# Optimization experiments

Measured on AMD Instinct MI355X. Metric: run time of the kernel, lower is better.

The kernel has to match this reference:

```python
import jax, jax.numpy as jnp
import numpy as np

N = 30000      # num nodes (cells)
E = 480000     # num edges (avg degree 16)
D_IN = 1000    # input_dim (genes)
H = 8          # nheads
F_H = 32       # hidden_dim per head
D_EMB = 64     # embedding_dim
NEG_SLOPE = 0.2


def setup_inputs() -> dict:
    key = jax.random.key(0)
    ks = jax.random.split(key, 12)
    glorot = lambda k, shape, fan: (jax.random.normal(k, shape, jnp.float32)
                                    * (1.0 / np.sqrt(fan)))
    return {
        "x": jax.random.normal(ks[0], (N, D_IN), jnp.float32),
        "edge_index": jax.random.randint(ks[1], (2, E), 0, N),
        "edge_weight": jax.random.uniform(ks[2], (E,), jnp.float32),
        # GATConv params
        "W": glorot(ks[3], (D_IN, H * F_H), D_IN),
        "att_src": glorot(ks[4], (H, F_H), F_H),
        "att_dst": glorot(ks[5], (H, F_H), F_H),
        "bias_gat": jnp.zeros((H * F_H,), jnp.float32),
        # embedding Linear
        "emb_W": glorot(ks[6], (H * F_H, D_EMB), H * F_H),
        "emb_b": jnp.zeros((D_EMB,), jnp.float32),
        # decoder MLP
        "dec_W1": glorot(ks[7], (D_EMB, F_H), D_EMB),
        "dec_b1": jnp.zeros((F_H,), jnp.float32),
        "dec_W2": glorot(ks[8], (F_H, D_IN), F_H),
        "dec_b2": jnp.zeros((D_IN,), jnp.float32),
    }


def _gat_conv(x, edge_index, W, att_src, att_dst, bias):
    n = x.shape[0]
    h = (x @ W).reshape(n, H, F_H)                    # [N,H,F]
    a_s = jnp.einsum('nhf,hf->nh', h, att_src)        # [N,H]
    a_d = jnp.einsum('nhf,hf->nh', h, att_dst)        # [N,H]
    # add self loops (PyG default add_self_loops=True)
    loops = jnp.arange(n)
    src = jnp.concatenate([edge_index[0], loops])     # [E+N]
    dst = jnp.concatenate([edge_index[1], loops])     # [E+N]
    logits = jax.nn.leaky_relu(a_s[src] + a_d[dst], NEG_SLOPE)  # [E+N,H]
    # segment softmax over incoming edges of each destination node
    m = jax.ops.segment_max(logits, dst, num_segments=n)        # [N,H]
    p = jnp.exp(logits - m[dst])
    denom = jax.ops.segment_sum(p, dst, num_segments=n)         # [N,H]
    alpha = p / denom[dst]                                      # [E+N,H]
    msg = h[src] * alpha[:, :, None]                            # [E+N,H,F]
    out = jax.ops.segment_sum(msg, dst, num_segments=n)         # [N,H,F]
    return out.reshape(n, H * F_H) + bias


def reference(x, edge_index, edge_weight, W, att_src, att_dst, bias_gat,
              emb_W, emb_b, dec_W1, dec_b1, dec_W2, dec_b2):
    # edge_weight is accepted but unused: PyG GATConv with edge_dim=None has
    # no edge-feature pathway.
    h = jax.nn.relu(_gat_conv(x, edge_index, W, att_src, att_dst, bias_gat))
    z = h @ emb_W + emb_b                               # [N, D_EMB]
    d = jax.nn.relu(z @ dec_W1 + dec_b1)                # [N, F_H]
    recon = d @ dec_W2 + dec_b2                         # [N, D_IN]
    return recon, z
```

## Files before the change

kernel.cpp:

```cpp
#include <hip/hip_runtime.h>
#include <hip/hip_bf16.h>

#define N_NODES 30000
#define N_EDGES 480000
#define D_IN    1000
#define KPAD    1024
#define NHEAD   8
#define F_HID   32
#define D_EMB   64
#define NEG_SLOPE 0.2f
#define MAXDEG  64

typedef __attribute__((ext_vector_type(4))) float  f32x4;
typedef __attribute__((ext_vector_type(8))) __bf16 bf16x8;
typedef __attribute__((ext_vector_type(4))) __bf16 bf16x4;

#define WT_TOT    (256*KPAD + D_EMB*256 + F_HID*D_EMB + D_IN*F_HID)
#define WT_BLOCKS ((WT_TOT + 255) / 256)
#define WA_BLOCKS (16 * KPAD / 256)
#define SC_CHUNK  4068
#define SC_BLOCKS (118 * 8)

__global__ __launch_bounds__(256) void cvt_w(
    const float* __restrict__ W, const float* __restrict__ emb_W,
    const float* __restrict__ d1, const float* __restrict__ d2,
    const float* __restrict__ att_src, const float* __restrict__ att_dst,
    __bf16* __restrict__ WbT, __bf16* __restrict__ embT,
    __bf16* __restrict__ d1T, __bf16* __restrict__ d2T,
    __bf16* __restrict__ WaT,
    const int* __restrict__ eidx, int* __restrict__ cnt,
    int* __restrict__ slots)
{
    int b = blockIdx.x;
    if (b < WT_BLOCKS) {
        int i = b * 256 + threadIdx.x;
        if (i < 256 * KPAD) {
            int n = i >> 10, k = i & 1023;
            WbT[i] = (k < D_IN) ? (__bf16)W[(size_t)k * 256 + n] : (__bf16)0.0f;
            return;
        }
        i -= 256 * KPAD;
        if (i < D_EMB * 256) {
            int n = i >> 8, k = i & 255;
            embT[i] = (__bf16)emb_W[(size_t)k * D_EMB + n];
            return;
        }
        i -= D_EMB * 256;
        if (i < F_HID * D_EMB) {
            int n = i >> 6, k = i & 63;
            d1T[i] = (__bf16)d1[(size_t)k * F_HID + n];
            return;
        }
        i -= F_HID * D_EMB;
        if (i < D_IN * F_HID) {
            int n = i >> 5, k = i & 31;
            d2T[i] = (__bf16)d2[(size_t)k * D_IN + n];
        }
        return;
    }
    b -= WT_BLOCKS;
    if (b < WA_BLOCKS) {
        int i = b * 256 + threadIdx.x;
        int j = i >> 10, k = i & 1023;
        float s = 0.f;
        if (k < D_IN) {
            const float* av = (j < 8 ? att_src : att_dst) + (j & 7) * F_HID;
            const float* wr = W + (size_t)k * 256 + (j & 7) * F_HID;
            #pragma unroll
            for (int f = 0; f < F_HID; f++) s += wr[f] * av[f];
        }
        WaT[i] = (__bf16)s;
        return;
    }
    b -= WA_BLOCKS;
    {
        const int shard = blockIdx.x & 7;
        const int chunk = b >> 3;
        int e0 = chunk * SC_CHUNK;
        int e1 = e0 + SC_CHUNK; if (e1 > N_EDGES) e1 = N_EDGES;
        for (int e = e0 + (int)threadIdx.x; e < e1; e += 256) {
            int d = eidx[N_EDGES + e];
            if (((d >> 4) & 7) == shard) {
                int slot = atomicAdd(&cnt[d], 1);
                slots[d * MAXDEG + slot] = eidx[e];
            }
        }
    }
}

__device__ __forceinline__ void stage_tile(
    __bf16* lds, const __bf16* __restrict__ g, int base, int maxr,
    int K, int k0, int rows, int w, int lane, int stride)
{
    const int rsub = lane >> 2;
    const int c    = lane & 3;
    for (int off = w * 1024; off < rows * 64; off += stride) {
        int r  = (off >> 6) + rsub;
        int gr = base + r; gr = gr > maxr ? maxr : gr;
        int chunk = c ^ (r & 3);
        const __bf16* gp = g + (size_t)gr * K + k0 + chunk * 8;
        __builtin_amdgcn_global_load_lds(
            (const __attribute__((address_space(1))) void*)gp,
            (__attribute__((address_space(3))) void*)((char*)lds + off),
            16, 0, 0);
    }
}

#define GEMM1_BLOCKS ((N_NODES + 63) / 64)

__device__ __forceinline__ void xload8(const float* __restrict__ xrow, int cb,
                                       f32x4& u0, f32x4& u1)
{
    if (cb < D_IN) {
        const f32x4* p = (const f32x4*)(xrow + cb);
        u0 = p[0]; u1 = p[1];
    } else {
        u0 = (f32x4){0.f, 0.f, 0.f, 0.f};
        u1 = (f32x4){0.f, 0.f, 0.f, 0.f};
    }
}

__device__ __forceinline__ bf16x8 cvt8(const f32x4& u0, const f32x4& u1)
{
    bf16x8 o;
    o[0] = (__bf16)u0.x; o[1] = (__bf16)u0.y; o[2] = (__bf16)u0.z; o[3] = (__bf16)u0.w;
    o[4] = (__bf16)u1.x; o[5] = (__bf16)u1.y; o[6] = (__bf16)u1.z; o[7] = (__bf16)u1.w;
    return o;
}

__global__ __launch_bounds__(512, 4) void gemm1_fused(
    const float* __restrict__ x, const __bf16* __restrict__ WbT,
    const __bf16* __restrict__ WaT, __bf16* __restrict__ hb,
    float* __restrict__ a_s, float* __restrict__ a_d, int M)
{
    __shared__ __align__(16) __bf16 As[2][64 * 32];
    __shared__ __align__(16) __bf16 Bs[2][256 * 32];

    const int tid  = threadIdx.x;
    const int w    = tid >> 6, lane = tid & 63;
    const int wm   = w >> 2,   wn   = w & 3;
    const int quad = lane >> 4, l16 = lane & 15;
    const int bm   = blockIdx.x * 64;

    const bool astage = (tid < 256);
    const int r0   = tid >> 2;
    const int cpos = tid & 3;
    const int cxor = (cpos ^ (r0 & 3)) << 3;
    int grow = bm + r0; if (grow > M - 1) grow = M - 1;
    const float* xrow = x + (size_t)grow * D_IN;

    const int brsub = lane >> 2;
    const int bc    = lane & 3;

    f32x4 acc[2][4];
    #pragma unroll
    for (int i = 0; i < 2; i++)
        #pragma unroll
        for (int j = 0; j < 4; j++)
            acc[i][j] = (f32x4){0.f, 0.f, 0.f, 0.f};
    f32x4 accA[2];
    #pragma unroll
    for (int i = 0; i < 2; i++) accA[i] = (f32x4){0.f, 0.f, 0.f, 0.f};

    const bool att = (wn == 0);
    const __bf16* warow = WaT + (size_t)l16 * KPAD + quad * 8;

    auto stageB = [&](int buf, int k0) {
        #pragma unroll
        for (int off = 0; off < 16384; off += 8192) {
            int o2 = off + w * 1024;
            int r = (o2 >> 6) + brsub;
            int chunk = bc ^ (r & 3);
            const __bf16* gp = WbT + (size_t)r * KPAD + k0 + chunk * 8;
            __builtin_amdgcn_global_load_lds(
                (const __attribute__((address_space(1))) void*)gp,
                (__attribute__((address_space(3))) void*)((char*)&Bs[buf][0] + o2),
                16, 0, 0);
        }
    };

    auto compute = [&](int buf, const bf16x8& attfrag) {
        bf16x8 af[2], bfr[4];
        #pragma unroll
        for (int mt = 0; mt < 2; mt++) {
            int r = wm * 32 + mt * 16 + l16;
            af[mt] = *(const bf16x8*)&As[buf][r * 32 + (quad ^ (r & 3)) * 8];
        }
        #pragma unroll
        for (int nt = 0; nt < 4; nt++) {
            int r = wn * 64 + nt * 16 + l16;
            bfr[nt] = *(const bf16x8*)&Bs[buf][r * 32 + (quad ^ (r & 3)) * 8];
        }
        #pragma unroll
        for (int mt = 0; mt < 2; mt++)
            #pragma unroll
            for (int nt = 0; nt < 4; nt++)
                acc[mt][nt] = __builtin_amdgcn_mfma_f32_16x16x32_bf16(
                    af[mt], bfr[nt], acc[mt][nt], 0, 0, 0);
        if (att) {
            #pragma unroll
            for (int mt = 0; mt < 2; mt++)
                accA[mt] = __builtin_amdgcn_mfma_f32_16x16x32_bf16(
                    af[mt], attfrag, accA[mt], 0, 0, 0);
        }
    };

    f32x4 x0, x1;
    if (astage) xload8(xrow, 0 + cxor, x0, x1);
    bf16x8 attc = {};
    if (att) attc = *(const bf16x8*)(warow + 0);
    stageB(0, 0);
    if (astage) *(bf16x8*)&As[0][r0 * 32 + cpos * 8] = cvt8(x0, x1);
    __syncthreads();

    #pragma unroll 2
    for (int p = 0; p < 32; ++p) {
        const int buf = p & 1;
        const int kn  = (p + 1) * 32;
        bf16x8 attn = {};
        if (p < 31) {
            if (astage) xload8(xrow, kn + cxor, x0, x1);
            if (att) attn = *(const bf16x8*)(warow + kn);
            stageB(buf ^ 1, kn);
        }
        compute(buf, attc);
        __builtin_amdgcn_sched_barrier(0);
        if (p < 31) {
            if (astage) *(bf16x8*)&As[buf ^ 1][r0 * 32 + cpos * 8] = cvt8(x0, x1);
        }
        attc = attn;
        __syncthreads();
    }

    #pragma unroll
    for (int nt = 0; nt < 4; nt++) {
        int col = wn * 64 + nt * 16 + l16;
        #pragma unroll
        for (int mt = 0; mt < 2; mt++) {
            int row0 = bm + wm * 32 + mt * 16 + quad * 4;
            #pragma unroll
            for (int rr = 0; rr < 4; rr++) {
                int row = row0 + rr;
                if (row < M)
                    hb[(size_t)row * 256 + col] = (__bf16)acc[mt][nt][rr];
            }
        }
    }
    if (att) {
        #pragma unroll
        for (int mt = 0; mt < 2; mt++) {
            int row0 = bm + wm * 32 + mt * 16 + quad * 4;
            #pragma unroll
            for (int rr = 0; rr < 4; rr++) {
                int row = row0 + rr;
                if (row < M) {
                    float v = accA[mt][rr];
                    if (l16 < 8) a_s[row * NHEAD + l16] = v;
                    else         a_d[row * NHEAD + (l16 - 8)] = v;
                }
            }
        }
    }
}

#define HROW 264

__device__ __forceinline__ float leaky(float x) {
    return x > 0.f ? x : NEG_SLOPE * x;
}

__global__ __launch_bounds__(512, 4) void gat_zdr(
    const __bf16* __restrict__ hb, const float* __restrict__ a_s,
    const float* __restrict__ a_d, const int* __restrict__ cnt,
    const int* __restrict__ slots, const float* __restrict__ bias,
    const __bf16* __restrict__ embT, const __bf16* __restrict__ d1T,
    const __bf16* __restrict__ d2T, const float* __restrict__ emb_b,
    const float* __restrict__ dec_b1, const float* __restrict__ dec_b2,
    float* __restrict__ z, float* __restrict__ recon, int M)
{
    __shared__ __align__(16) __bf16 hgatS[64 * HROW];
    __shared__ __align__(16) __bf16 Bs[64 * 32];
    __shared__ __align__(16) __bf16 zS[64 * 64];
    __shared__ __align__(16) __bf16 Bs2[2 * 32 * 32];
    __shared__ __align__(16) __bf16 dS[64 * 32];

    const int tid  = threadIdx.x;
    const int wv   = tid >> 6, lane = tid & 63;
    const int quad = lane >> 4, l16 = lane & 15;
    const int bm   = blockIdx.x * 64;

    stage_tile(Bs2,        d1T, 0, 31, 64, 0,  32, wv, lane, 4096);
    stage_tile(Bs2 + 1024, d1T, 0, 31, 64, 32, 32, wv, lane, 4096);

    {
        const int hh = lane >> 3;
        const int fo = (lane & 7) * 4;
        const f32x4 bv = *(const f32x4*)(bias + lane * 4);
        for (int i = 0; i < 8; i++) {
            int n = bm + wv * 8 + i;
            if (n >= M) break;
            const int base = n * MAXDEG;
            const int c = cnt[n];
            const float adn = a_d[n * NHEAD + hh];

            float p = __expf(leaky(a_s[n * NHEAD + hh] + adn));
            float denom = p;
            f32x4 acc;
            {
                bf16x4 hv = *(const bf16x4*)(hb + (size_t)n * 256 + hh * F_HID + fo);
                acc.x = p * (float)hv[0]; acc.y = p * (float)hv[1];
                acc.z = p * (float)hv[2]; acc.w = p * (float)hv[3];
            }
            int e = 0;
            for (; e + 8 <= c; e += 8) {
                const int4 sA = *(const int4*)(slots + base + e);
                const int4 sB = *(const int4*)(slots + base + e + 4);
                float l0 = a_s[sA.x * NHEAD + hh], l1 = a_s[sA.y * NHEAD + hh];
                float l2 = a_s[sA.z * NHEAD + hh], l3 = a_s[sA.w * NHEAD + hh];
                float l4 = a_s[sB.x * NHEAD + hh], l5 = a_s[sB.y * NHEAD + hh];
                float l6 = a_s[sB.z * NHEAD + hh], l7 = a_s[sB.w * NHEAD + hh];
                bf16x4 h0 = *(const bf16x4*)(hb + (size_t)sA.x * 256 + hh * F_HID + fo);
                bf16x4 h1 = *(const bf16x4*)(hb + (size_t)sA.y * 256 + hh * F_HID + fo);
                bf16x4 h2 = *(const bf16x4*)(hb + (size_t)sA.z * 256 + hh * F_HID + fo);
                bf16x4 h3 = *(const bf16x4*)(hb + (size_t)sA.w * 256 + hh * F_HID + fo);
                bf16x4 h4 = *(const bf16x4*)(hb + (size_t)sB.x * 256 + hh * F_HID + fo);
                bf16x4 h5 = *(const bf16x4*)(hb + (size_t)sB.y * 256 + hh * F_HID + fo);
                bf16x4 h6 = *(const bf16x4*)(hb + (size_t)sB.z * 256 + hh * F_HID + fo);
                bf16x4 h7 = *(const bf16x4*)(hb + (size_t)sB.w * 256 + hh * F_HID + fo);
                float p0 = __expf(leaky(l0 + adn)), p1 = __expf(leaky(l1 + adn));
                float p2 = __expf(leaky(l2 + adn)), p3 = __expf(leaky(l3 + adn));
                float p4 = __expf(leaky(l4 + adn)), p5 = __expf(leaky(l5 + adn));
                float p6 = __expf(leaky(l6 + adn)), p7 = __expf(leaky(l7 + adn));
                denom += ((p0 + p1) + (p2 + p3)) + ((p4 + p5) + (p6 + p7));
                acc.x += p0*(float)h0[0] + p1*(float)h1[0] + p2*(float)h2[0] + p3*(float)h3[0]
                       + p4*(float)h4[0] + p5*(float)h5[0] + p6*(float)h6[0] + p7*(float)h7[0];
                acc.y += p0*(float)h0[1] + p1*(float)h1[1] + p2*(float)h2[1] + p3*(float)h3[1]
                       + p4*(float)h4[1] + p5*(float)h5[1] + p6*(float)h6[1] + p7*(float)h7[1];
                acc.z += p0*(float)h0[2] + p1*(float)h1[2] + p2*(float)h2[2] + p3*(float)h3[2]
                       + p4*(float)h4[2] + p5*(float)h5[2] + p6*(float)h6[2] + p7*(float)h7[2];
                acc.w += p0*(float)h0[3] + p1*(float)h1[3] + p2*(float)h2[3] + p3*(float)h3[3]
                       + p4*(float)h4[3] + p5*(float)h5[3] + p6*(float)h6[3] + p7*(float)h7[3];
            }
            for (; e + 4 <= c; e += 4) {
                const int4 ss = *(const int4*)(slots + base + e);
                float l0 = a_s[ss.x * NHEAD + hh], l1 = a_s[ss.y * NHEAD + hh];
                float l2 = a_s[ss.z * NHEAD + hh], l3 = a_s[ss.w * NHEAD + hh];
                bf16x4 h0 = *(const bf16x4*)(hb + (size_t)ss.x * 256 + hh * F_HID + fo);
                bf16x4 h1 = *(const bf16x4*)(hb + (size_t)ss.y * 256 + hh * F_HID + fo);
                bf16x4 h2 = *(const bf16x4*)(hb + (size_t)ss.z * 256 + hh * F_HID + fo);
                bf16x4 h3 = *(const bf16x4*)(hb + (size_t)ss.w * 256 + hh * F_HID + fo);
                float p0 = __expf(leaky(l0 + adn)), p1 = __expf(leaky(l1 + adn));
                float p2 = __expf(leaky(l2 + adn)), p3 = __expf(leaky(l3 + adn));
                denom += (p0 + p1) + (p2 + p3);
                acc.x += p0*(float)h0[0] + p1*(float)h1[0] + p2*(float)h2[0] + p3*(float)h3[0];
                acc.y += p0*(float)h0[1] + p1*(float)h1[1] + p2*(float)h2[1] + p3*(float)h3[1];
                acc.z += p0*(float)h0[2] + p1*(float)h1[2] + p2*(float)h2[2] + p3*(float)h3[2];
                acc.w += p0*(float)h0[3] + p1*(float)h1[3] + p2*(float)h2[3] + p3*(float)h3[3];
            }
            for (; e < c; e++) {
                int s = slots[base + e];
                float pe = __expf(leaky(a_s[s * NHEAD + hh] + adn));
                denom += pe;
                bf16x4 hv = *(const bf16x4*)(hb + (size_t)s * 256 + hh * F_HID + fo);
                acc.x += pe * (float)hv[0]; acc.y += pe * (float)hv[1];
                acc.z += pe * (float)hv[2]; acc.w += pe * (float)hv[3];
            }
            float inv = 1.0f / denom;
            float o0 = acc.x * inv + bv.x, o1 = acc.y * inv + bv.y;
            float o2 = acc.z * inv + bv.z, o3 = acc.w * inv + bv.w;
            o0 = o0 > 0.f ? o0 : 0.f;
            o1 = o1 > 0.f ? o1 : 0.f;
            o2 = o2 > 0.f ? o2 : 0.f;
            o3 = o3 > 0.f ? o3 : 0.f;
            bf16x4 ob;
            ob[0] = (__bf16)o0; ob[1] = (__bf16)o1; ob[2] = (__bf16)o2; ob[3] = (__bf16)o3;
            *(bf16x4*)&hgatS[(wv * 8 + i) * HROW + lane * 4] = ob;
        }
    }
    __syncthreads();

    const int wm  = wv >> 2;
    const int wn4 = wv & 3;
    f32x4 acc[2];
    acc[0] = (f32x4){0,0,0,0}; acc[1] = (f32x4){0,0,0,0};

    for (int k0 = 0; k0 < 256; k0 += 32) {
        stage_tile(Bs, embT, 0, D_EMB - 1, 256, k0, 64, wv, lane, 4096);
        __syncthreads();
        bf16x8 af[2], bfr;
        #pragma unroll
        for (int mt = 0; mt < 2; mt++) {
            int r = wm * 32 + mt * 16 + l16;
            af[mt] = *(const bf16x8*)&hgatS[r * HROW + k0 + quad * 8];
        }
        {
            int r = wn4 * 16 + l16;
            bfr = *(const bf16x8*)&Bs[r * 32 + (quad ^ (r & 3)) * 8];
        }
        #pragma unroll
        for (int mt = 0; mt < 2; mt++)
            acc[mt] = __builtin_amdgcn_mfma_f32_16x16x32_bf16(af[mt], bfr, acc[mt], 0, 0, 0);
        __syncthreads();
    }

    {
        int col = wn4 * 16 + l16;
        float bv = emb_b[col];
        int t = col >> 5, cch = (col >> 3) & 3, j = col & 7;
        #pragma unroll
        for (int mt = 0; mt < 2; mt++) {
            int rl0 = wm * 32 + mt * 16 + quad * 4;
            #pragma unroll
            for (int rr = 0; rr < 4; rr++) {
                int rl = rl0 + rr;
                int row = bm + rl;
                float v = acc[mt][rr] + bv;
                if (row < M) z[(size_t)row * D_EMB + col] = v;
                zS[t * 2048 + rl * 32 + (cch ^ (rl & 3)) * 8 + j] = (__bf16)v;
            }
        }
    }
    __syncthreads();

    if (wn4 < 2) {
        f32x4 accd[2];
        accd[0] = (f32x4){0,0,0,0}; accd[1] = (f32x4){0,0,0,0};
        #pragma unroll
        for (int t = 0; t < 2; t++) {
            bf16x8 af[2], bfr;
            #pragma unroll
            for (int mt = 0; mt < 2; mt++) {
                int r = wm * 32 + mt * 16 + l16;
                af[mt] = *(const bf16x8*)&zS[t * 2048 + r * 32 + (quad ^ (r & 3)) * 8];
            }
            {
                int r = wn4 * 16 + l16;
                bfr = *(const bf16x8*)&Bs2[t * 1024 + r * 32 + (quad ^ (r & 3)) * 8];
            }
            #pragma unroll
            for (int mt = 0; mt < 2; mt++)
                accd[mt] = __builtin_amdgcn_mfma_f32_16x16x32_bf16(af[mt], bfr, accd[mt], 0, 0, 0);
        }
        int col = wn4 * 16 + l16;
        float bv = dec_b1[col];
        int cc = col >> 3, j = col & 7;
        #pragma unroll
        for (int mt = 0; mt < 2; mt++) {
            int rl0 = wm * 32 + mt * 16 + quad * 4;
            #pragma unroll
            for (int rr = 0; rr < 4; rr++) {
                int rl = rl0 + rr;
                float v = accd[mt][rr] + bv;
                v = v > 0.f ? v : 0.f;
                dS[rl * 32 + (cc ^ (rl & 3)) * 8 + j] = (__bf16)v;
            }
        }
    }
    __syncthreads();

    {
        const int wtt = wv & 3;
        bf16x8 daf[2];
        #pragma unroll
        for (int mt = 0; mt < 2; mt++) {
            int r = wm * 32 + mt * 16 + l16;
            daf[mt] = *(const bf16x8*)&dS[r * 32 + (quad ^ (r & 3)) * 8];
        }
        for (int tt = wtt; tt < 63; tt += 4) {
            int crow = tt * 16 + l16;
            if (crow > D_IN - 1) crow = D_IN - 1;
            bf16x8 bfr = *(const bf16x8*)&d2T[(size_t)crow * 32 + quad * 8];
            f32x4 a[2];
            #pragma unroll
            for (int mt = 0; mt < 2; mt++) {
                a[mt] = (f32x4){0.f, 0.f, 0.f, 0.f};
                a[mt] = __builtin_amdgcn_mfma_f32_16x16x32_bf16(bfr, daf[mt], a[mt], 0, 0, 0);
            }
            int col0 = tt * 16 + quad * 4;
            if (col0 + 3 < D_IN) {
                f32x4 bv = *(const f32x4*)&dec_b2[col0];
                #pragma unroll
                for (int mt = 0; mt < 2; mt++) {
                    int row = bm + wm * 32 + mt * 16 + l16;
                    if (row < M) {
                        f32x4 o;
                        o.x = a[mt].x + bv.x; o.y = a[mt].y + bv.y;
                        o.z = a[mt].z + bv.z; o.w = a[mt].w + bv.w;
                        *(f32x4*)&recon[(size_t)row * D_IN + col0] = o;
                    }
                }
            }
        }
    }
}

extern "C" void kernel_launch(void* const* d_in, const int* in_sizes, int n_in,
                              void* d_out, int out_size, void* d_ws, size_t ws_size,
                              hipStream_t stream)
{
    const float* x        = (const float*)d_in[0];
    const int*   eidx     = (const int*)  d_in[1];
    const float* W        = (const float*)d_in[3];
    const float* att_src  = (const float*)d_in[4];
    const float* att_dst  = (const float*)d_in[5];
    const float* bias_gat = (const float*)d_in[6];
    const float* emb_W    = (const float*)d_in[7];
    const float* emb_b    = (const float*)d_in[8];
    const float* dec_W1   = (const float*)d_in[9];
    const float* dec_b1   = (const float*)d_in[10];
    const float* dec_W2   = (const float*)d_in[11];
    const float* dec_b2   = (const float*)d_in[12];

    float* out   = (float*)d_out;
    float* recon = out;
    float* z     = out + (size_t)N_NODES * D_IN;

    char* ws = (char*)d_ws;
    size_t o = 0;
    auto alloc = [&](size_t bytes) { char* p = ws + o; o = (o + bytes + 255) & ~(size_t)255; return p; };
    __bf16* hb      = (__bf16*)alloc((size_t)N_NODES * 256 * 2);
    __bf16* WbT     = (__bf16*)alloc((size_t)256 * KPAD * 2);
    __bf16* embT    = (__bf16*)alloc((size_t)D_EMB * 256 * 2);
    __bf16* d1T     = (__bf16*)alloc((size_t)F_HID * D_EMB * 2);
    __bf16* d2T     = (__bf16*)alloc((size_t)D_IN * F_HID * 2);
    __bf16* WaT     = (__bf16*)alloc((size_t)16 * KPAD * 2);
    float*  a_s     = (float*) alloc((size_t)N_NODES * NHEAD * 4);
    float*  a_d     = (float*) alloc((size_t)N_NODES * NHEAD * 4);
    int*    slots   = (int*)   alloc((size_t)N_NODES * MAXDEG * 4);
    int*    cnt     = (int*)   alloc((size_t)N_NODES * 4);

    hipMemsetAsync(cnt, 0, (size_t)N_NODES * 4, stream);

    cvt_w<<<WT_BLOCKS + WA_BLOCKS + SC_BLOCKS, 256, 0, stream>>>(
        W, emb_W, dec_W1, dec_W2, att_src, att_dst,
        WbT, embT, d1T, d2T, WaT, eidx, cnt, slots);

    gemm1_fused<<<GEMM1_BLOCKS, 512, 0, stream>>>(
        x, WbT, WaT, hb, a_s, a_d, N_NODES);

    gat_zdr<<<GEMM1_BLOCKS, 512, 0, stream>>>(
        hb, a_s, a_d, cnt, slots, bias_gat,
        embT, d1T, d2T, emb_b, dec_b1, dec_b2, z, recon, N_NODES);
}
```

Before: 355.3 us.

## Tile W transpose via LDS and interleave two-node gathers in GAT aggregation

The W-to-bf16 transpose moves from per-element strided reads to 64x64 LDS-tiled blocks, so both global reads and writes are coalesced. The GAT aggregation now processes two destination nodes per wave iteration and interleaves their 4-edge gathers, putting more independent memory loads in flight to hide gather latency. In exchange the loop uses more registers and has extra tail loops for uneven degrees.

```diff
diff --git a/kernel.cpp b/kernel.cpp
--- a/kernel.cpp
+++ b/kernel.cpp
@@ -15,11 +15,12 @@
 typedef __attribute__((ext_vector_type(8))) __bf16 bf16x8;
 typedef __attribute__((ext_vector_type(4))) __bf16 bf16x4;
 
-#define WT_TOT    (256*KPAD + D_EMB*256 + F_HID*D_EMB + D_IN*F_HID)
-#define WT_BLOCKS ((WT_TOT + 255) / 256)
-#define WA_BLOCKS (16 * KPAD / 256)
-#define SC_CHUNK  4068
-#define SC_BLOCKS (118 * 8)
+#define WBT_TILES   64
+#define REST_TOT    (D_EMB*256 + F_HID*D_EMB + D_IN*F_HID)
+#define REST_BLOCKS ((REST_TOT + 255) / 256)
+#define WA_BLOCKS   (16 * KPAD / 256)
+#define SC_CHUNK    4068
+#define SC_BLOCKS   (118 * 8)
 
 __global__ __launch_bounds__(256) void cvt_w(
     const float* __restrict__ W, const float* __restrict__ emb_W,
@@ -32,14 +33,29 @@
     int* __restrict__ slots)
 {
     int b = blockIdx.x;
-    if (b < WT_BLOCKS) {
+    if (b < WBT_TILES) {
+        __shared__ float tile[64][65];
+        const int kt = b >> 2, nt = b & 3;
+        const int k0 = kt * 64, n0 = nt * 64;
+        const int r = threadIdx.x >> 6;
+        const int c = threadIdx.x & 63;
+        #pragma unroll
+        for (int j = 0; j < 16; j++) {
+            int row = j * 4 + r;
+            int k = k0 + row;
+            tile[row][c] = (k < D_IN) ? W[(size_t)k * 256 + n0 + c] : 0.0f;
+        }
+        __syncthreads();
+        #pragma unroll
+        for (int j = 0; j < 16; j++) {
+            int nrow = j * 4 + r;
+            WbT[(size_t)(n0 + nrow) * KPAD + k0 + c] = (__bf16)tile[c][nrow];
+        }
+        return;
+    }
+    b -= WBT_TILES;
+    if (b < REST_BLOCKS) {
         int i = b * 256 + threadIdx.x;
-        if (i < 256 * KPAD) {
-            int n = i >> 10, k = i & 1023;
-            WbT[i] = (k < D_IN) ? (__bf16)W[(size_t)k * 256 + n] : (__bf16)0.0f;
-            return;
-        }
-        i -= 256 * KPAD;
         if (i < D_EMB * 256) {
             int n = i >> 8, k = i & 255;
             embT[i] = (__bf16)emb_W[(size_t)k * D_EMB + n];
@@ -58,7 +74,7 @@
         }
         return;
     }
-    b -= WT_BLOCKS;
+    b -= REST_BLOCKS;
     if (b < WA_BLOCKS) {
         int i = b * 256 + threadIdx.x;
         int j = i >> 10, k = i & 1023;
@@ -296,85 +312,102 @@
         const int hh = lane >> 3;
         const int fo = (lane & 7) * 4;
         const f32x4 bv = *(const f32x4*)(bias + lane * 4);
-        for (int i = 0; i < 8; i++) {
-            int n = bm + wv * 8 + i;
-            if (n >= M) break;
-            const int base = n * MAXDEG;
-            const int c = cnt[n];
-            const float adn = a_d[n * NHEAD + hh];
-
-            float p = __expf(leaky(a_s[n * NHEAD + hh] + adn));
-            float denom = p;
-            f32x4 acc;
+
+        auto gather4 = [&](int base, int e, float adn, f32x4& acc, float& denom) {
+            const int4 ss = *(const int4*)(slots + base + e);
+            float l0 = a_s[ss.x * NHEAD + hh], l1 = a_s[ss.y * NHEAD + hh];
+            float l2 = a_s[ss.z * NHEAD + hh], l3 = a_s[ss.w * NHEAD + hh];
+            bf16x4 h0 = *(const bf16x4*)(hb + (size_t)ss.x * 256 + hh * F_HID + fo);
+            bf16x4 h1 = *(const bf16x4*)(hb + (size_t)ss.y * 256 + hh * F_HID + fo);
+            bf16x4 h2 = *(const bf16x4*)(hb + (size_t)ss.z * 256 + hh * F_HID + fo);
+            bf16x4 h3 = *(const bf16x4*)(hb + (size_t)ss.w * 256 + hh * F_HID + fo);
+            float p0 = __expf(leaky(l0 + adn)), p1 = __expf(leaky(l1 + adn));
+            float p2 = __expf(leaky(l2 + adn)), p3 = __expf(leaky(l3 + adn));
+            denom += (p0 + p1) + (p2 + p3);
+            acc.x += p0*(float)h0[0] + p1*(float)h1[0] + p2*(float)h2[0] + p3*(float)h3[0];
+            acc.y += p0*(float)h0[1] + p1*(float)h1[1] + p2*(float)h2[1] + p3*(float)h3[1];
+            acc.z += p0*(float)h0[2] + p1*(float)h1[2] + p2*(float)h2[2] + p3*(float)h3[2];
+            acc.w += p0*(float)h0[3] + p1*(float)h1[3] + p2*(float)h2[3] + p3*(float)h3[3];
+        };
+        auto gather1 = [&](int base, int e, float adn, f32x4& acc, float& denom) {
+            int s = slots[base + e];
+            float pe = __expf(leaky(a_s[s * NHEAD + hh] + adn));
+            denom += pe;
+            bf16x4 hv = *(const bf16x4*)(hb + (size_t)s * 256 + hh * F_HID + fo);
+            acc.x += pe * (float)hv[0]; acc.y += pe * (float)hv[1];
+            acc.z += pe * (float)hv[2]; acc.w += pe * (float)hv[3];
+        };
+
+        #pragma unroll
+        for (int i = 0; i < 4; i++) {
+            const int nA = bm + wv * 8 + i * 2;
+            const int nB = nA + 1;
+            const bool vA = nA < M, vB = nB < M;
+            const int iA = vA ? nA : M - 1;
+            const int iB = vB ? nB : M - 1;
+            const int baseA = iA * MAXDEG, baseB = iB * MAXDEG;
+            const int cA = vA ? cnt[iA] : 0;
+            const int cB = vB ? cnt[iB] : 0;
+            const float adnA = a_d[iA * NHEAD + hh];
+            const float adnB = a_d[iB * NHEAD + hh];
+
+            float pA = __expf(leaky(a_s[iA * NHEAD + hh] + adnA));
+            float pB = __expf(leaky(a_s[iB * NHEAD + hh] + adnB));
+            float denA = pA, denB = pB;
+            f32x4 accA, accB;
             {
-                bf16x4 hv = *(const bf16x4*)(hb + (size_t)n * 256 + hh * F_HID + fo);
-                acc.x = p * (float)hv[0]; acc.y = p * (float)hv[1];
-                acc.z = p * (float)hv[2]; acc.w = p * (float)hv[3];
-            }
-            int e = 0;
-            for (; e + 8 <= c; e += 8) {
-                const int4 sA = *(const int4*)(slots + base + e);
-                const int4 sB = *(const int4*)(slots + base + e + 4);
-                float l0 = a_s[sA.x * NHEAD + hh], l1 = a_s[sA.y * NHEAD + hh];
-                float l2 = a_s[sA.z * NHEAD + hh], l3 = a_s[sA.w * NHEAD + hh];
-                float l4 = a_s[sB.x * NHEAD + hh], l5 = a_s[sB.y * NHEAD + hh];
-                float l6 = a_s[sB.z * NHEAD + hh], l7 = a_s[sB.w * NHEAD + hh];
-                bf16x4 h0 = *(const bf16x4*)(hb + (size_t)sA.x * 256 + hh * F_HID + fo);
-                bf16x4 h1 = *(const bf16x4*)(hb + (size_t)sA.y * 256 + hh * F_HID + fo);
-                bf16x4 h2 = *(const bf16x4*)(hb + (size_t)sA.z * 256 + hh * F_HID + fo);
-                bf16x4 h3 = *(const bf16x4*)(hb + (size_t)sA.w * 256 + hh * F_HID + fo);
-                bf16x4 h4 = *(const bf16x4*)(hb + (size_t)sB.x * 256 + hh * F_HID + fo);
-                bf16x4 h5 = *(const bf16x4*)(hb + (size_t)sB.y * 256 + hh * F_HID + fo);
-                bf16x4 h6 = *(const bf16x4*)(hb + (size_t)sB.z * 256 + hh * F_HID + fo);
-                bf16x4 h7 = *(const bf16x4*)(hb + (size_t)sB.w * 256 + hh * F_HID + fo);
-                float p0 = __expf(leaky(l0 + adn)), p1 = __expf(leaky(l1 + adn));
-                float p2 = __expf(leaky(l2 + adn)), p3 = __expf(leaky(l3 + adn));
-                float p4 = __expf(leaky(l4 + adn)), p5 = __expf(leaky(l5 + adn));
-                float p6 = __expf(leaky(l6 + adn)), p7 = __expf(leaky(l7 + adn));
-                denom += ((p0 + p1) + (p2 + p3)) + ((p4 + p5) + (p6 + p7));
-                acc.x += p0*(float)h0[0] + p1*(float)h1[0] + p2*(float)h2[0] + p3*(float)h3[0]
-                       + p4*(float)h4[0] + p5*(float)h5[0] + p6*(float)h6[0] + p7*(float)h7[0];
-                acc.y += p0*(float)h0[1] + p1*(float)h1[1] + p2*(float)h2[1] + p3*(float)h3[1]
-                       + p4*(float)h4[1] + p5*(float)h5[1] + p6*(float)h6[1] + p7*(float)h7[1];
-                acc.z += p0*(float)h0[2] + p1*(float)h1[2] + p2*(float)h2[2] + p3*(float)h3[2]
-                       + p4*(float)h4[2] + p5*(float)h5[2] + p6*(float)h6[2] + p7*(float)h7[2];
-                acc.w += p0*(float)h0[3] + p1*(float)h1[3] + p2*(float)h2[3] + p3*(float)h3[3]
-                       + p4*(float)h4[3] + p5*(float)h5[3] + p6*(float)h6[3] + p7*(float)h7[3];
-            }
-            for (; e + 4 <= c; e += 4) {
-                const int4 ss = *(const int4*)(slots + base + e);
-                float l0 = a_s[ss.x * NHEAD + hh], l1 = a_s[ss.y * NHEAD + hh];
-                float l2 = a_s[ss.z * NHEAD + hh], l3 = a_s[ss.w * NHEAD + hh];
-                bf16x4 h0 = *(const bf16x4*)(hb + (size_t)ss.x * 256 + hh * F_HID + fo);
-                bf16x4 h1 = *(const bf16x4*)(hb + (size_t)ss.y * 256 + hh * F_HID + fo);
-                bf16x4 h2 = *(const bf16x4*)(hb + (size_t)ss.z * 256 + hh * F_HID + fo);
-                bf16x4 h3 = *(const bf16x4*)(hb + (size_t)ss.w * 256 + hh * F_HID + fo);
-                float p0 = __expf(leaky(l0 + adn)), p1 = __expf(leaky(l1 + adn));
-                float p2 = __expf(leaky(l2 + adn)), p3 = __expf(leaky(l3 + adn));
-                denom += (p0 + p1) + (p2 + p3);
-                acc.x += p0*(float)h0[0] + p1*(float)h1[0] + p2*(float)h2[0] + p3*(float)h3[0];
-                acc.y += p0*(float)h0[1] + p1*(float)h1[1] + p2*(float)h2[1] + p3*(float)h3[1];
-                acc.z += p0*(float)h0[2] + p1*(float)h1[2] + p2*(float)h2[2] + p3*(float)h3[2];
-                acc.w += p0*(float)h0[3] + p1*(float)h1[3] + p2*(float)h2[3] + p3*(float)h3[3];
-            }
-            for (; e < c; e++) {
-                int s = slots[base + e];
-                float pe = __expf(leaky(a_s[s * NHEAD + hh] + adn));
-                denom += pe;
-                bf16x4 hv = *(const bf16x4*)(hb + (size_t)s * 256 + hh * F_HID + fo);
-                acc.x += pe * (float)hv[0]; acc.y += pe * (float)hv[1];
-                acc.z += pe * (float)hv[2]; acc.w += pe * (float)hv[3];
-            }
-            float inv = 1.0f / denom;
-            float o0 = acc.x * inv + bv.x, o1 = acc.y * inv + bv.y;
-            float o2 = acc.z * inv + bv.z, o3 = acc.w * inv + bv.w;
-            o0 = o0 > 0.f ? o0 : 0.f;
-            o1 = o1 > 0.f ? o1 : 0.f;
-            o2 = o2 > 0.f ? o2 : 0.f;
-            o3 = o3 > 0.f ? o3 : 0.f;
-            bf16x4 ob;
-            ob[0] = (__bf16)o0; ob[1] = (__bf16)o1; ob[2] = (__bf16)o2; ob[3] = (__bf16)o3;
-            *(bf16x4*)&hgatS[(wv * 8 + i) * HROW + lane * 4] = ob;
+                bf16x4 hvA = *(const bf16x4*)(hb + (size_t)iA * 256 + hh * F_HID + fo);
+                bf16x4 hvB = *(const bf16x4*)(hb + (size_t)iB * 256 + hh * F_HID + fo);
+                accA.x = pA*(float)hvA[0]; accA.y = pA*(float)hvA[1];
+                accA.z = pA*(float)hvA[2]; accA.w = pA*(float)hvA[3];
+                accB.x = pB*(float)hvB[0]; accB.y = pB*(float)hvB[1];
+                accB.z = pB*(float)hvB[2]; accB.w = pB*(float)hvB[3];
+            }
+            int eA = 0, eB = 0;
+            while (eA + 8 <= cA && eB + 8 <= cB) {
+                gather4(baseA, eA,     adnA, accA, denA);
+                gather4(baseB, eB,     adnB, accB, denB);
+                gather4(baseA, eA + 4, adnA, accA, denA);
+                gather4(baseB, eB + 4, adnB, accB, denB);
+                eA += 8; eB += 8;
+            }
+            while (eA + 8 <= cA) {
+                gather4(baseA, eA, adnA, accA, denA);
+                gather4(baseA, eA + 4, adnA, accA, denA);
+                eA += 8;
+            }
+            while (eB + 8 <= cB) {
+                gather4(baseB, eB, adnB, accB, denB);
+                gather4(baseB, eB + 4, adnB, accB, denB);
+                eB += 8;
+            }
+            if (eA + 4 <= cA) { gather4(baseA, eA, adnA, accA, denA); eA += 4; }
+            if (eB + 4 <= cB) { gather4(baseB, eB, adnB, accB, denB); eB += 4; }
+            for (; eA < cA; eA++) gather1(baseA, eA, adnA, accA, denA);
+            for (; eB < cB; eB++) gather1(baseB, eB, adnB, accB, denB);
+
+            if (vA) {
+                float inv = 1.0f / denA;
+                float o0 = accA.x * inv + bv.x, o1 = accA.y * inv + bv.y;
+                float o2 = accA.z * inv + bv.z, o3 = accA.w * inv + bv.w;
+                o0 = o0 > 0.f ? o0 : 0.f; o1 = o1 > 0.f ? o1 : 0.f;
+                o2 = o2 > 0.f ? o2 : 0.f; o3 = o3 > 0.f ? o3 : 0.f;
+                bf16x4 ob;
+                ob[0] = (__bf16)o0; ob[1] = (__bf16)o1;
+                ob[2] = (__bf16)o2; ob[3] = (__bf16)o3;
+                *(bf16x4*)&hgatS[(wv * 8 + i * 2) * HROW + lane * 4] = ob;
+            }
+            if (vB) {
+                float inv = 1.0f / denB;
+                float o0 = accB.x * inv + bv.x, o1 = accB.y * inv + bv.y;
+                float o2 = accB.z * inv + bv.z, o3 = accB.w * inv + bv.w;
+                o0 = o0 > 0.f ? o0 : 0.f; o1 = o1 > 0.f ? o1 : 0.f;
+                o2 = o2 > 0.f ? o2 : 0.f; o3 = o3 > 0.f ? o3 : 0.f;
+                bf16x4 ob;
+                ob[0] = (__bf16)o0; ob[1] = (__bf16)o1;
+                ob[2] = (__bf16)o2; ob[3] = (__bf16)o3;
+                *(bf16x4*)&hgatS[(wv * 8 + i * 2 + 1) * HROW + lane * 4] = ob;
+            }
         }
     }
     __syncthreads();
@@ -531,7 +564,7 @@
 
     hipMemsetAsync(cnt, 0, (size_t)N_NODES * 4, stream);
 
-    cvt_w<<<WT_BLOCKS + WA_BLOCKS + SC_BLOCKS, 256, 0, stream>>>(
+    cvt_w<<<WBT_TILES + REST_BLOCKS + WA_BLOCKS + SC_BLOCKS, 256, 0, stream>>>(
         W, emb_W, dec_W1, dec_W2, att_src, att_dst,
         WbT, embT, d1T, d2T, WaT, eidx, cnt, slots);
 
```

After: 350.7 us. No clear change (-1.3%).
